# Performance work log

Hardware: AMD Instinct MI355X
Metric: run time of the kernel (lower is better)

The kernel has to match this reference:

```python
import jax, jax.numpy as jnp
import numpy as np

E = 8          # num_experts
TOP_K = 2      # router top-k
ALPHA = 1.702  # swigluoai alpha
LIMIT = 7.0    # swigluoai clamp limit


def setup_inputs() -> dict:
    key = jax.random.key(0)
    ks = jax.random.split(key, 7)
    B, S, H, I = 2, 1024, 1024, 1024
    s = 1.0 / np.sqrt(H)  # keep activations O(1), realistic init scale
    return {
        "x": jax.random.normal(ks[0], (B, S, H), jnp.float32),
        "router_weight": jax.random.normal(ks[1], (E, H), jnp.float32) * s,
        "router_bias": jax.random.normal(ks[2], (E,), jnp.float32) * 0.01,
        "w1": jax.random.normal(ks[3], (E, H, 2 * I), jnp.float32) * s,  # interleaved gate/up
        "w1_bias": jax.random.normal(ks[4], (E, 2 * I), jnp.float32) * 0.01,
        "w2": jax.random.normal(ks[5], (E, I, H), jnp.float32) * s,
        "w2_bias": jax.random.normal(ks[6], (E, H), jnp.float32) * 0.01,
    }


def _moe(x, router_weight, router_bias, w1, w1_bias, w2, w2_bias):
    B, S, H = x.shape
    xf = x.reshape(-1, H)                                   # [T, H]
    # ---- router: softmax over expert logits, then top-k ----
    logits = xf @ router_weight.T + router_bias             # [T, E]
    probs = jax.nn.softmax(logits, axis=-1)
    expert_weights, expert_ids = jax.lax.top_k(probs, TOP_K)  # [T, k]
    # combine weights scattered to dense [T, E] (no normalization: normalize_expert_weights=None)
    combine = jnp.sum(jax.nn.one_hot(expert_ids, E, dtype=xf.dtype)
                      * expert_weights[..., None], axis=1)  # [T, E]
    # ---- grouped MLP, expressed densely per expert (reference semantics) ----
    h = jnp.einsum('th,ehi->eti', xf, w1) + w1_bias[:, None, :]   # [E, T, 2I]
    gate = h[..., 0::2]                                          # interleaved layout
    up = h[..., 1::2]
    gate = jnp.minimum(gate, LIMIT)                              # swigluoai: clamp gate max
    up = jnp.clip(up, -LIMIT, LIMIT)                             # clamp up both sides
    glu = gate * jax.nn.sigmoid(gate * ALPHA)
    act = (up + 1.0) * glu                                       # [E, T, I]
    y = jnp.einsum('eti,eih->eth', act, w2) + w2_bias[:, None, :]  # [E, T, H]
    out = jnp.einsum('eth,te->th', y, combine)                   # weighted combine
    return out.reshape(B, S, H), expert_weights


def reference(x, router_weight, router_bias, w1, w1_bias, w2, w2_bias):
    return _moe(x, router_weight, router_bias, w1, w1_bias, w2, w2_bias)
```

## Files before the change

### kernel.cpp

```cpp
#include <hip/hip_runtime.h>
#include <cstdint>
#include <cstddef>

typedef unsigned short u16;
typedef short bf16x8 __attribute__((ext_vector_type(8)));
typedef float floatx4 __attribute__((ext_vector_type(4)));

#define GLD16(gp, sp) __builtin_amdgcn_global_load_lds(                      \
    (const __attribute__((address_space(1))) void*)(gp),                     \
    (__attribute__((address_space(3))) void*)(sp), 16, 0, 0)

__device__ __forceinline__ u16 f2bf(float f) {
  unsigned u = __float_as_uint(f);
  u += 0x7fffu + ((u >> 16) & 1u);
  return (u16)(u >> 16);
}

__global__ void cvt_x_kernel(const float4* __restrict__ in, u16* __restrict__ out, int n4) {
  int i = blockIdx.x * blockDim.x + threadIdx.x;
  if (i >= n4) return;
  float4 v = in[i];
  ushort4 o;
  o.x = f2bf(v.x); o.y = f2bf(v.y); o.z = f2bf(v.z); o.w = f2bf(v.w);
  ((ushort4*)out)[i] = o;
}

__global__ void transpose_cvt_kernel(const float* __restrict__ in, u16* __restrict__ out,
                                     int R, int C) {
  __shared__ float tile[32][33];
  size_t base = (size_t)blockIdx.z * (size_t)R * (size_t)C;
  int c0 = blockIdx.x * 32, r0 = blockIdx.y * 32;
  int tx = threadIdx.x, ty = threadIdx.y;
#pragma unroll
  for (int k = 0; k < 32; k += 8)
    tile[ty + k][tx] = in[base + (size_t)(r0 + ty + k) * C + (c0 + tx)];
  __syncthreads();
#pragma unroll
  for (int k = 0; k < 32; k += 8)
    out[base + (size_t)(c0 + ty + k) * R + (r0 + tx)] = f2bf(tile[tx][ty + k]);
}

__global__ void router_kernel(const float* __restrict__ x, const float* __restrict__ rw,
                              const float* __restrict__ rb, float* __restrict__ ew,
                              int* __restrict__ eids, float* __restrict__ eprobs) {
  const int wave = threadIdx.x >> 6, lane = threadIdx.x & 63;
  const int t = blockIdx.x * 4 + wave;
  const float4* xv = (const float4*)(x + (size_t)t * 1024);
  float acc[8];
#pragma unroll
  for (int e = 0; e < 8; ++e) acc[e] = 0.f;
  for (int j = lane; j < 256; j += 64) {
    float4 xx = xv[j];
#pragma unroll
    for (int e = 0; e < 8; ++e) {
      float4 wv = ((const float4*)(rw + (size_t)e * 1024))[j];
      acc[e] += xx.x * wv.x + xx.y * wv.y + xx.z * wv.z + xx.w * wv.w;
    }
  }
#pragma unroll
  for (int e = 0; e < 8; ++e) {
    float v = acc[e];
#pragma unroll
    for (int off = 32; off > 0; off >>= 1) v += __shfl_down(v, off);
    acc[e] = v;
  }
  if (lane == 0) {
    float p[8];
    float mx = -1e30f;
#pragma unroll
    for (int e = 0; e < 8; ++e) { p[e] = acc[e] + rb[e]; mx = fmaxf(mx, p[e]); }
    float sum = 0.f;
#pragma unroll
    for (int e = 0; e < 8; ++e) { p[e] = __expf(p[e] - mx); sum += p[e]; }
    float inv = 1.f / sum;
#pragma unroll
    for (int e = 0; e < 8; ++e) p[e] *= inv;
    int i0 = 0;
#pragma unroll
    for (int e = 1; e < 8; ++e) if (p[e] > p[i0]) i0 = e;
    int i1 = (i0 == 0) ? 1 : 0;
#pragma unroll
    for (int e = 0; e < 8; ++e) if (e != i0 && e != i1 && p[e] > p[i1]) i1 = e;
    ew[t * 2 + 0] = p[i0];
    ew[t * 2 + 1] = p[i1];
    eids[t * 2 + 0] = i0;
    eids[t * 2 + 1] = i1;
    eprobs[t * 2 + 0] = p[i0];
    eprobs[t * 2 + 1] = p[i1];
  }
}

__global__ void build_lists_kernel(const int* __restrict__ eids, const float* __restrict__ eprobs,
                                   int* __restrict__ row_token, float* __restrict__ row_scale,
                                   int* __restrict__ meta) {
  __shared__ int cnt[8], base[8], cur[8];
  const int tid = threadIdx.x;
  if (tid < 8) { cnt[tid] = 0; cur[tid] = 0; }
  __syncthreads();
  for (int t = tid; t < 2048; t += 256) {
    atomicAdd(&cnt[eids[t * 2 + 0]], 1);
    atomicAdd(&cnt[eids[t * 2 + 1]], 1);
  }
  __syncthreads();
  if (tid == 0) {
    int off = 0, w = 0;
    for (int e = 0; e < 8; ++e) {
      base[e] = off;
      meta[48 + e] = off;
      int nb = (cnt[e] + 127) >> 7;
      for (int rb = 0; rb < nb; ++rb) meta[1 + w++] = (e << 8) | rb;
      off += nb << 7;
    }
    meta[0] = w;
  }
  __syncthreads();
  for (int s = tid; s < 5120; s += 256) { row_token[s] = -1; row_scale[s] = 0.f; }
  __syncthreads();
  for (int t = tid; t < 2048; t += 256) {
#pragma unroll
    for (int k = 0; k < 2; ++k) {
      int e = eids[t * 2 + k];
      int s = base[e] + atomicAdd(&cur[e], 1);
      row_token[s] = t;
      row_scale[s] = eprobs[t * 2 + k];
    }
  }
}

__global__ void bias_init_kernel(const int* __restrict__ eids, const float* __restrict__ eprobs,
                                 const float* __restrict__ w2b, float* __restrict__ out) {
  int idx = blockIdx.x * 256 + threadIdx.x;
  int t = idx >> 10, h = idx & 1023;
  int e0 = eids[t * 2], e1 = eids[t * 2 + 1];
  out[idx] = eprobs[t * 2] * w2b[e0 * 1024 + h] + eprobs[t * 2 + 1] * w2b[e1 * 1024 + h];
}

__global__ __launch_bounds__(256) void gemm1_act_kernel(
    const u16* __restrict__ xb, const u16* __restrict__ w1t,
    const float* __restrict__ w1b,
    const int* __restrict__ row_token, const float* __restrict__ row_scale,
    const int* __restrict__ meta, u16* __restrict__ actS) {
  if ((int)blockIdx.x >= meta[0]) return;
  __shared__ __align__(16) u16 As[128 * 32];
  __shared__ __align__(16) u16 Bs[128 * 32];
  const int w = meta[1 + blockIdx.x];
  const int e = w >> 8, rb = w & 255;
  const int slotB = meta[48 + e] + rb * 128;
  const int colBase = blockIdx.y * 128;
  const int tid = threadIdx.x, lane = tid & 63, wave = tid >> 6;
  const int row16 = lane & 15, chunk = lane >> 4;
  const u16* Bt = w1t + (size_t)e * 2048 * 1024;
  const u16* aP[2]; const u16* bP[2];
#pragma unroll
  for (int r = 0; r < 2; ++r) {
    int g = r * 4 + wave;
    int tk = row_token[slotB + g * 16 + row16];
    if (tk < 0) tk = 0;
    aP[r] = xb + (size_t)tk * 1024 + chunk * 8;
    bP[r] = Bt + (size_t)(colBase + g * 16 + row16) * 1024 + chunk * 8;
  }
  const int wr = wave >> 1, wc = wave & 1;
  floatx4 acc[4][4];
#pragma unroll
  for (int mi = 0; mi < 4; ++mi)
#pragma unroll
    for (int ni = 0; ni < 4; ++ni) acc[mi][ni] = floatx4{0.f, 0.f, 0.f, 0.f};

  for (int kt = 0; kt < 32; ++kt) {
    const int k = kt * 32;
    GLD16(aP[0] + k, As + wave * 512);
    GLD16(bP[0] + k, Bs + wave * 512);
    GLD16(aP[1] + k, As + (4 + wave) * 512);
    GLD16(bP[1] + k, Bs + (4 + wave) * 512);
    __syncthreads();
    bf16x8 af[4], bfr[4];
#pragma unroll
    for (int mi = 0; mi < 4; ++mi) af[mi] = *(const bf16x8*)(As + (wr * 4 + mi) * 512 + lane * 8);
#pragma unroll
    for (int ni = 0; ni < 4; ++ni) bfr[ni] = *(const bf16x8*)(Bs + (wc * 4 + ni) * 512 + lane * 8);
#pragma unroll
    for (int mi = 0; mi < 4; ++mi)
#pragma unroll
      for (int ni = 0; ni < 4; ++ni)
        acc[mi][ni] = __builtin_amdgcn_mfma_f32_16x16x32_bf16(af[mi], bfr[ni], acc[mi][ni], 0, 0, 0);
    __syncthreads();
  }

  const int cl = lane & 15, ql = lane >> 4;
#pragma unroll
  for (int mi = 0; mi < 4; ++mi) {
#pragma unroll
    for (int r = 0; r < 4; ++r) {
      const int slot = slotB + wr * 64 + mi * 16 + ql * 4 + r;
      const float c = row_scale[slot];
#pragma unroll
      for (int ni = 0; ni < 4; ++ni) {
        const int n = colBase + wc * 64 + ni * 16 + cl;
        float v = acc[mi][ni][r] + w1b[e * 2048 + n];
        float o = __shfl_xor(v, 1);
        if ((lane & 1) == 0) {
          float g = fminf(v, 7.f);
          float u = fminf(fmaxf(o, -7.f), 7.f);
          float sg = 1.f / (1.f + __expf(-1.702f * g));
          float a = (u + 1.f) * (g * sg);
          actS[(size_t)slot * 1024 + (n >> 1)] = f2bf(c * a);
        }
      }
    }
  }
}

__global__ __launch_bounds__(256) void gemm2_add_kernel(
    const u16* __restrict__ actS, const u16* __restrict__ w2t,
    const int* __restrict__ row_token, const int* __restrict__ meta,
    float* __restrict__ out) {
  if ((int)blockIdx.x >= meta[0]) return;
  __shared__ __align__(16) u16 As[128 * 32];
  __shared__ __align__(16) u16 Bs[128 * 32];
  const int w = meta[1 + blockIdx.x];
  const int e = w >> 8, rb = w & 255;
  const int slotB = meta[48 + e] + rb * 128;
  const int colBase = blockIdx.y * 128;
  const int tid = threadIdx.x, lane = tid & 63, wave = tid >> 6;
  const int row16 = lane & 15, chunk = lane >> 4;
  const u16* Bt = w2t + (size_t)e * 1024 * 1024;
  const u16* aP[2]; const u16* bP[2];
#pragma unroll
  for (int r = 0; r < 2; ++r) {
    int g = r * 4 + wave;
    aP[r] = actS + (size_t)(slotB + g * 16 + row16) * 1024 + chunk * 8;
    bP[r] = Bt + (size_t)(colBase + g * 16 + row16) * 1024 + chunk * 8;
  }
  const int wr = wave >> 1, wc = wave & 1;
  floatx4 acc[4][4];
#pragma unroll
  for (int mi = 0; mi < 4; ++mi)
#pragma unroll
    for (int ni = 0; ni < 4; ++ni) acc[mi][ni] = floatx4{0.f, 0.f, 0.f, 0.f};

  for (int kt = 0; kt < 32; ++kt) {
    const int k = kt * 32;
    GLD16(aP[0] + k, As + wave * 512);
    GLD16(bP[0] + k, Bs + wave * 512);
    GLD16(aP[1] + k, As + (4 + wave) * 512);
    GLD16(bP[1] + k, Bs + (4 + wave) * 512);
    __syncthreads();
    bf16x8 af[4], bfr[4];
#pragma unroll
    for (int mi = 0; mi < 4; ++mi) af[mi] = *(const bf16x8*)(As + (wr * 4 + mi) * 512 + lane * 8);
#pragma unroll
    for (int ni = 0; ni < 4; ++ni) bfr[ni] = *(const bf16x8*)(Bs + (wc * 4 + ni) * 512 + lane * 8);
#pragma unroll
    for (int mi = 0; mi < 4; ++mi)
#pragma unroll
      for (int ni = 0; ni < 4; ++ni)
        acc[mi][ni] = __builtin_amdgcn_mfma_f32_16x16x32_bf16(af[mi], bfr[ni], acc[mi][ni], 0, 0, 0);
    __syncthreads();
  }

  const int cl = lane & 15, ql = lane >> 4;
#pragma unroll
  for (int mi = 0; mi < 4; ++mi)
#pragma unroll
    for (int r = 0; r < 4; ++r) {
      const int slot = slotB + wr * 64 + mi * 16 + ql * 4 + r;
      const int tok = row_token[slot];
      if (tok < 0) continue;
#pragma unroll
      for (int ni = 0; ni < 4; ++ni) {
        const int col = colBase + wc * 64 + ni * 16 + cl;
        atomicAdd(out + (size_t)tok * 1024 + col, acc[mi][ni][r]);
      }
    }
}

extern "C" void kernel_launch(void* const* d_in, const int* in_sizes, int n_in,
                              void* d_out, int out_size, void* d_ws, size_t ws_size,
                              hipStream_t stream) {
  const float* x   = (const float*)d_in[0];
  const float* rw  = (const float*)d_in[1];
  const float* rb  = (const float*)d_in[2];
  const float* w1  = (const float*)d_in[3];
  const float* w1b = (const float*)d_in[4];
  const float* w2  = (const float*)d_in[5];
  const float* w2b = (const float*)d_in[6];
  float* out = (float*)d_out;
  float* ew  = out + (size_t)2048 * 1024;

  char* ws = (char*)d_ws;
  u16* xb        = (u16*)(ws);
  u16* w1t       = (u16*)(ws + (4ull << 20));
  u16* w2t       = (u16*)(ws + (36ull << 20));
  u16* actS      = (u16*)(ws + (52ull << 20));
  int* eids      = (int*)(ws + (62ull << 20));
  float* eprobs  = (float*)(ws + (62ull << 20) + (16 << 10));
  int* row_token = (int*)(ws + (62ull << 20) + (32 << 10));
  float* row_scale = (float*)(ws + (62ull << 20) + (52 << 10));
  int* meta      = (int*)(ws + (62ull << 20) + (72 << 10));

  cvt_x_kernel<<<2048, 256, 0, stream>>>((const float4*)x, xb, 2048 * 1024 / 4);
  transpose_cvt_kernel<<<dim3(64, 32, 8), dim3(32, 8), 0, stream>>>(w1, w1t, 1024, 2048);
  transpose_cvt_kernel<<<dim3(32, 32, 8), dim3(32, 8), 0, stream>>>(w2, w2t, 1024, 1024);
  router_kernel<<<512, 256, 0, stream>>>(x, rw, rb, ew, eids, eprobs);
  build_lists_kernel<<<1, 256, 0, stream>>>(eids, eprobs, row_token, row_scale, meta);
  bias_init_kernel<<<8192, 256, 0, stream>>>(eids, eprobs, w2b, out);
  gemm1_act_kernel<<<dim3(40, 16), 256, 0, stream>>>(xb, w1t, w1b, row_token, row_scale, meta, actS);
  gemm2_add_kernel<<<dim3(40, 8), 256, 0, stream>>>(actS, w2t, row_token, meta, out);
}
```

Measured before the change: 272.6 us.

## Triple-buffer GEMM loads, fuse x cast into router, replace atomics with combine

Both expert GEMMs now use a three-stage LDS ring buffer with explicit vmcnt waits and scheduling barriers, so global-to-LDS loads overlap MFMA work. MFMA priority is raised during compute. The x-to-bf16 conversion moves into the router kernel, removing one launch and one read of x. GEMM2 uses narrower 64-column tiles and writes per-slot results to a scratch buffer, and a new combine kernel gathers the two expert rows per token plus the bias, replacing float atomics. This costs an extra fp32 intermediate write and read, and the intermediate reuses the w1t workspace region after GEMM1 has finished with it.

```diff
diff --git a/kernel.cpp b/kernel.cpp
--- a/kernel.cpp
+++ b/kernel.cpp
@@ -9,20 +9,19 @@
 #define GLD16(gp, sp) __builtin_amdgcn_global_load_lds(                      \
     (const __attribute__((address_space(1))) void*)(gp),                     \
     (__attribute__((address_space(3))) void*)(sp), 16, 0, 0)
+
+#define VWAIT(N) asm volatile("s_waitcnt vmcnt(" #N ")" ::: "memory")
+#define BARF()                                                               \
+  do {                                                                       \
+    __builtin_amdgcn_sched_barrier(0);                                       \
+    __builtin_amdgcn_s_barrier();                                            \
+    __builtin_amdgcn_sched_barrier(0);                                       \
+  } while (0)
 
 __device__ __forceinline__ u16 f2bf(float f) {
   unsigned u = __float_as_uint(f);
   u += 0x7fffu + ((u >> 16) & 1u);
   return (u16)(u >> 16);
-}
-
-__global__ void cvt_x_kernel(const float4* __restrict__ in, u16* __restrict__ out, int n4) {
-  int i = blockIdx.x * blockDim.x + threadIdx.x;
-  if (i >= n4) return;
-  float4 v = in[i];
-  ushort4 o;
-  o.x = f2bf(v.x); o.y = f2bf(v.y); o.z = f2bf(v.z); o.w = f2bf(v.w);
-  ((ushort4*)out)[i] = o;
 }
 
 __global__ void transpose_cvt_kernel(const float* __restrict__ in, u16* __restrict__ out,
@@ -42,15 +41,20 @@
 
 __global__ void router_kernel(const float* __restrict__ x, const float* __restrict__ rw,
                               const float* __restrict__ rb, float* __restrict__ ew,
-                              int* __restrict__ eids, float* __restrict__ eprobs) {
+                              int* __restrict__ eids, float* __restrict__ eprobs,
+                              u16* __restrict__ xb) {
   const int wave = threadIdx.x >> 6, lane = threadIdx.x & 63;
   const int t = blockIdx.x * 4 + wave;
   const float4* xv = (const float4*)(x + (size_t)t * 1024);
+  ushort4* xo = (ushort4*)(xb + (size_t)t * 1024);
   float acc[8];
 #pragma unroll
   for (int e = 0; e < 8; ++e) acc[e] = 0.f;
   for (int j = lane; j < 256; j += 64) {
     float4 xx = xv[j];
+    ushort4 o;
+    o.x = f2bf(xx.x); o.y = f2bf(xx.y); o.z = f2bf(xx.z); o.w = f2bf(xx.w);
+    xo[j] = o;
 #pragma unroll
     for (int e = 0; e < 8; ++e) {
       float4 wv = ((const float4*)(rw + (size_t)e * 1024))[j];
@@ -92,7 +96,7 @@
 
 __global__ void build_lists_kernel(const int* __restrict__ eids, const float* __restrict__ eprobs,
                                    int* __restrict__ row_token, float* __restrict__ row_scale,
-                                   int* __restrict__ meta) {
+                                   int* __restrict__ tok2slot, int* __restrict__ meta) {
   __shared__ int cnt[8], base[8], cur[8];
   const int tid = threadIdx.x;
   if (tid < 8) { cnt[tid] = 0; cur[tid] = 0; }
@@ -123,16 +127,25 @@
       int s = base[e] + atomicAdd(&cur[e], 1);
       row_token[s] = t;
       row_scale[s] = eprobs[t * 2 + k];
-    }
-  }
-}
-
-__global__ void bias_init_kernel(const int* __restrict__ eids, const float* __restrict__ eprobs,
-                                 const float* __restrict__ w2b, float* __restrict__ out) {
-  int idx = blockIdx.x * 256 + threadIdx.x;
-  int t = idx >> 10, h = idx & 1023;
-  int e0 = eids[t * 2], e1 = eids[t * 2 + 1];
-  out[idx] = eprobs[t * 2] * w2b[e0 * 1024 + h] + eprobs[t * 2 + 1] * w2b[e1 * 1024 + h];
+      tok2slot[t * 2 + k] = s;
+    }
+  }
+}
+
+__device__ __forceinline__ void g1_compute(const u16* AsR, const u16* BsR, int wr, int wc,
+                                           int lane, floatx4 (&acc)[4][4]) {
+  bf16x8 af[4], bfr[4];
+#pragma unroll
+  for (int mi = 0; mi < 4; ++mi) af[mi] = *(const bf16x8*)(AsR + (wr * 4 + mi) * 512 + lane * 8);
+#pragma unroll
+  for (int ni = 0; ni < 4; ++ni) bfr[ni] = *(const bf16x8*)(BsR + (wc * 4 + ni) * 512 + lane * 8);
+  __builtin_amdgcn_s_setprio(1);
+#pragma unroll
+  for (int mi = 0; mi < 4; ++mi)
+#pragma unroll
+    for (int ni = 0; ni < 4; ++ni)
+      acc[mi][ni] = __builtin_amdgcn_mfma_f32_16x16x32_bf16(af[mi], bfr[ni], acc[mi][ni], 0, 0, 0);
+  __builtin_amdgcn_s_setprio(0);
 }
 
 __global__ __launch_bounds__(256) void gemm1_act_kernel(
@@ -141,8 +154,8 @@
     const int* __restrict__ row_token, const float* __restrict__ row_scale,
     const int* __restrict__ meta, u16* __restrict__ actS) {
   if ((int)blockIdx.x >= meta[0]) return;
-  __shared__ __align__(16) u16 As[128 * 32];
-  __shared__ __align__(16) u16 Bs[128 * 32];
+  __shared__ __align__(16) u16 As[3][128 * 32];
+  __shared__ __align__(16) u16 Bs[3][128 * 32];
   const int w = meta[1 + blockIdx.x];
   const int e = w >> 8, rb = w & 255;
   const int slotB = meta[48 + e] + rb * 128;
@@ -166,25 +179,32 @@
 #pragma unroll
     for (int ni = 0; ni < 4; ++ni) acc[mi][ni] = floatx4{0.f, 0.f, 0.f, 0.f};
 
-  for (int kt = 0; kt < 32; ++kt) {
-    const int k = kt * 32;
-    GLD16(aP[0] + k, As + wave * 512);
-    GLD16(bP[0] + k, Bs + wave * 512);
-    GLD16(aP[1] + k, As + (4 + wave) * 512);
-    GLD16(bP[1] + k, Bs + (4 + wave) * 512);
-    __syncthreads();
-    bf16x8 af[4], bfr[4];
-#pragma unroll
-    for (int mi = 0; mi < 4; ++mi) af[mi] = *(const bf16x8*)(As + (wr * 4 + mi) * 512 + lane * 8);
-#pragma unroll
-    for (int ni = 0; ni < 4; ++ni) bfr[ni] = *(const bf16x8*)(Bs + (wc * 4 + ni) * 512 + lane * 8);
-#pragma unroll
-    for (int mi = 0; mi < 4; ++mi)
-#pragma unroll
-      for (int ni = 0; ni < 4; ++ni)
-        acc[mi][ni] = __builtin_amdgcn_mfma_f32_16x16x32_bf16(af[mi], bfr[ni], acc[mi][ni], 0, 0, 0);
-    __syncthreads();
-  }
+#define G1_STAGE(W, KT)                                                      \
+  {                                                                          \
+    const int kk = (KT) * 32;                                                \
+    GLD16(aP[0] + kk, As[W] + wave * 512);                                   \
+    GLD16(bP[0] + kk, Bs[W] + wave * 512);                                   \
+    GLD16(aP[1] + kk, As[W] + (4 + wave) * 512);                             \
+    GLD16(bP[1] + kk, Bs[W] + (4 + wave) * 512);                             \
+  }
+
+  G1_STAGE(0, 0);
+  G1_STAGE(1, 1);
+
+#pragma unroll 1
+  for (int kt = 0; kt < 30; kt += 3) {
+    G1_STAGE(2, kt + 2); VWAIT(8); BARF();
+    g1_compute(As[0], Bs[0], wr, wc, lane, acc); BARF();
+    G1_STAGE(0, kt + 3); VWAIT(8); BARF();
+    g1_compute(As[1], Bs[1], wr, wc, lane, acc); BARF();
+    G1_STAGE(1, kt + 4); VWAIT(8); BARF();
+    g1_compute(As[2], Bs[2], wr, wc, lane, acc); BARF();
+  }
+  VWAIT(4); BARF();
+  g1_compute(As[0], Bs[0], wr, wc, lane, acc); BARF();
+  VWAIT(0); BARF();
+  g1_compute(As[1], Bs[1], wr, wc, lane, acc);
+#undef G1_STAGE
 
   const int cl = lane & 15, ql = lane >> 4;
 #pragma unroll
@@ -210,53 +230,74 @@
   }
 }
 
-__global__ __launch_bounds__(256) void gemm2_add_kernel(
+__device__ __forceinline__ void g2_compute(const u16* AsR, const u16* BsR, int wr, int wc,
+                                           int lane, floatx4 (&acc)[4][2]) {
+  bf16x8 af[4], bfr[2];
+#pragma unroll
+  for (int mi = 0; mi < 4; ++mi) af[mi] = *(const bf16x8*)(AsR + (wr * 4 + mi) * 512 + lane * 8);
+#pragma unroll
+  for (int ni = 0; ni < 2; ++ni) bfr[ni] = *(const bf16x8*)(BsR + (wc * 2 + ni) * 512 + lane * 8);
+  __builtin_amdgcn_s_setprio(1);
+#pragma unroll
+  for (int mi = 0; mi < 4; ++mi)
+#pragma unroll
+    for (int ni = 0; ni < 2; ++ni)
+      acc[mi][ni] = __builtin_amdgcn_mfma_f32_16x16x32_bf16(af[mi], bfr[ni], acc[mi][ni], 0, 0, 0);
+  __builtin_amdgcn_s_setprio(0);
+}
+
+__global__ __launch_bounds__(256) void gemm2_kernel(
     const u16* __restrict__ actS, const u16* __restrict__ w2t,
-    const int* __restrict__ row_token, const int* __restrict__ meta,
-    float* __restrict__ out) {
+    const int* __restrict__ meta, float* __restrict__ y) {
   if ((int)blockIdx.x >= meta[0]) return;
-  __shared__ __align__(16) u16 As[128 * 32];
-  __shared__ __align__(16) u16 Bs[128 * 32];
+  __shared__ __align__(16) u16 As[3][128 * 32];
+  __shared__ __align__(16) u16 Bs[3][64 * 32];
   const int w = meta[1 + blockIdx.x];
   const int e = w >> 8, rb = w & 255;
   const int slotB = meta[48 + e] + rb * 128;
-  const int colBase = blockIdx.y * 128;
+  const int colBase = blockIdx.y * 64;
   const int tid = threadIdx.x, lane = tid & 63, wave = tid >> 6;
   const int row16 = lane & 15, chunk = lane >> 4;
   const u16* Bt = w2t + (size_t)e * 1024 * 1024;
-  const u16* aP[2]; const u16* bP[2];
+  const u16* aP[2]; const u16* bP1;
 #pragma unroll
   for (int r = 0; r < 2; ++r) {
     int g = r * 4 + wave;
     aP[r] = actS + (size_t)(slotB + g * 16 + row16) * 1024 + chunk * 8;
-    bP[r] = Bt + (size_t)(colBase + g * 16 + row16) * 1024 + chunk * 8;
-  }
+  }
+  bP1 = Bt + (size_t)(colBase + wave * 16 + row16) * 1024 + chunk * 8;
   const int wr = wave >> 1, wc = wave & 1;
-  floatx4 acc[4][4];
-#pragma unroll
-  for (int mi = 0; mi < 4; ++mi)
-#pragma unroll
-    for (int ni = 0; ni < 4; ++ni) acc[mi][ni] = floatx4{0.f, 0.f, 0.f, 0.f};
-
-  for (int kt = 0; kt < 32; ++kt) {
-    const int k = kt * 32;
-    GLD16(aP[0] + k, As + wave * 512);
-    GLD16(bP[0] + k, Bs + wave * 512);
-    GLD16(aP[1] + k, As + (4 + wave) * 512);
-    GLD16(bP[1] + k, Bs + (4 + wave) * 512);
-    __syncthreads();
-    bf16x8 af[4], bfr[4];
-#pragma unroll
-    for (int mi = 0; mi < 4; ++mi) af[mi] = *(const bf16x8*)(As + (wr * 4 + mi) * 512 + lane * 8);
-#pragma unroll
-    for (int ni = 0; ni < 4; ++ni) bfr[ni] = *(const bf16x8*)(Bs + (wc * 4 + ni) * 512 + lane * 8);
-#pragma unroll
-    for (int mi = 0; mi < 4; ++mi)
-#pragma unroll
-      for (int ni = 0; ni < 4; ++ni)
-        acc[mi][ni] = __builtin_amdgcn_mfma_f32_16x16x32_bf16(af[mi], bfr[ni], acc[mi][ni], 0, 0, 0);
-    __syncthreads();
-  }
+  floatx4 acc[4][2];
+#pragma unroll
+  for (int mi = 0; mi < 4; ++mi)
+#pragma unroll
+    for (int ni = 0; ni < 2; ++ni) acc[mi][ni] = floatx4{0.f, 0.f, 0.f, 0.f};
+
+#define G2_STAGE(W, KT)                                                      \
+  {                                                                          \
+    const int kk = (KT) * 32;                                                \
+    GLD16(aP[0] + kk, As[W] + wave * 512);                                   \
+    GLD16(aP[1] + kk, As[W] + (4 + wave) * 512);                             \
+    GLD16(bP1 + kk, Bs[W] + wave * 512);                                     \
+  }
+
+  G2_STAGE(0, 0);
+  G2_STAGE(1, 1);
+
+#pragma unroll 1
+  for (int kt = 0; kt < 30; kt += 3) {
+    G2_STAGE(2, kt + 2); VWAIT(6); BARF();
+    g2_compute(As[0], Bs[0], wr, wc, lane, acc); BARF();
+    G2_STAGE(0, kt + 3); VWAIT(6); BARF();
+    g2_compute(As[1], Bs[1], wr, wc, lane, acc); BARF();
+    G2_STAGE(1, kt + 4); VWAIT(6); BARF();
+    g2_compute(As[2], Bs[2], wr, wc, lane, acc); BARF();
+  }
+  VWAIT(3); BARF();
+  g2_compute(As[0], Bs[0], wr, wc, lane, acc); BARF();
+  VWAIT(0); BARF();
+  g2_compute(As[1], Bs[1], wr, wc, lane, acc);
+#undef G2_STAGE
 
   const int cl = lane & 15, ql = lane >> 4;
 #pragma unroll
@@ -264,14 +305,23 @@
 #pragma unroll
     for (int r = 0; r < 4; ++r) {
       const int slot = slotB + wr * 64 + mi * 16 + ql * 4 + r;
-      const int tok = row_token[slot];
-      if (tok < 0) continue;
-#pragma unroll
-      for (int ni = 0; ni < 4; ++ni) {
-        const int col = colBase + wc * 64 + ni * 16 + cl;
-        atomicAdd(out + (size_t)tok * 1024 + col, acc[mi][ni][r]);
+#pragma unroll
+      for (int ni = 0; ni < 2; ++ni) {
+        const int col = colBase + wc * 32 + ni * 16 + cl;
+        y[(size_t)slot * 1024 + col] = acc[mi][ni][r];
       }
     }
+}
+
+__global__ void combine_kernel(const float* __restrict__ y, const int* __restrict__ eids,
+                               const float* __restrict__ eprobs, const int* __restrict__ tok2slot,
+                               const float* __restrict__ w2b, float* __restrict__ out) {
+  int idx = blockIdx.x * 256 + threadIdx.x;
+  int t = idx >> 10, h = idx & 1023;
+  int e0 = eids[t * 2], e1 = eids[t * 2 + 1];
+  int s0 = tok2slot[t * 2], s1 = tok2slot[t * 2 + 1];
+  out[idx] = eprobs[t * 2] * w2b[e0 * 1024 + h] + eprobs[t * 2 + 1] * w2b[e1 * 1024 + h]
+           + y[(size_t)s0 * 1024 + h] + y[(size_t)s1 * 1024 + h];
 }
 
 extern "C" void kernel_launch(void* const* d_in, const int* in_sizes, int n_in,
@@ -290,6 +340,7 @@
   char* ws = (char*)d_ws;
   u16* xb        = (u16*)(ws);
   u16* w1t       = (u16*)(ws + (4ull << 20));
+  float* y       = (float*)(ws + (4ull << 20));
   u16* w2t       = (u16*)(ws + (36ull << 20));
   u16* actS      = (u16*)(ws + (52ull << 20));
   int* eids      = (int*)(ws + (62ull << 20));
@@ -297,13 +348,13 @@
   int* row_token = (int*)(ws + (62ull << 20) + (32 << 10));
   float* row_scale = (float*)(ws + (62ull << 20) + (52 << 10));
   int* meta      = (int*)(ws + (62ull << 20) + (72 << 10));
-
-  cvt_x_kernel<<<2048, 256, 0, stream>>>((const float4*)x, xb, 2048 * 1024 / 4);
+  int* tok2slot  = (int*)(ws + (62ull << 20) + (74 << 10));
+
   transpose_cvt_kernel<<<dim3(64, 32, 8), dim3(32, 8), 0, stream>>>(w1, w1t, 1024, 2048);
   transpose_cvt_kernel<<<dim3(32, 32, 8), dim3(32, 8), 0, stream>>>(w2, w2t, 1024, 1024);
-  router_kernel<<<512, 256, 0, stream>>>(x, rw, rb, ew, eids, eprobs);
-  build_lists_kernel<<<1, 256, 0, stream>>>(eids, eprobs, row_token, row_scale, meta);
-  bias_init_kernel<<<8192, 256, 0, stream>>>(eids, eprobs, w2b, out);
+  router_kernel<<<512, 256, 0, stream>>>(x, rw, rb, ew, eids, eprobs, xb);
+  build_lists_kernel<<<1, 256, 0, stream>>>(eids, eprobs, row_token, row_scale, tok2slot, meta);
   gemm1_act_kernel<<<dim3(40, 16), 256, 0, stream>>>(xb, w1t, w1b, row_token, row_scale, meta, actS);
-  gemm2_add_kernel<<<dim3(40, 8), 256, 0, stream>>>(actS, w2t, row_token, meta, out);
-}
+  gemm2_kernel<<<dim3(40, 16), 256, 0, stream>>>(actS, w2t, meta, y);
+  combine_kernel<<<8192, 256, 0, stream>>>(y, eids, eprobs, tok2slot, w2b, out);
+}
```

Result: faster. 262.5 us (-3.7%).
